# Optimization experiments

Measured on AMD Instinct MI355X. Metric: run time of the kernel, lower is better.

The kernel has to match this reference:

```python
import jax, jax.numpy as jnp
import numpy as np

N_LAYERS = 24  # number of recurrent applications of the shared HashLinear


def setup_inputs() -> dict:
    key = jax.random.key(0)
    ks = jax.random.split(key, 9)
    B, D_IN, N, N_OUT = 1024, 784, 4096, 10
    s_in = 1.0 / np.sqrt(D_IN)
    s_h = 1.0 / np.sqrt(N)
    x = jax.random.normal(ks[0], (B, D_IN), jnp.float32)
    # nn.Linear(prod(input_dim), 2*n_units)
    W_in = jax.random.uniform(ks[1], (2 * N, D_IN), jnp.float32, -s_in, s_in)
    b_in = jax.random.uniform(ks[2], (2 * N,), jnp.float32, -s_in, s_in)
    # HashLinear(n_units, n_units, period=1, 'hash'): learnable +/-1 context key + shared linear
    key_sp = jnp.where(jax.random.bernoulli(ks[3], 0.5, (1, N)), 1.0, -1.0).astype(jnp.float32)
    W_sp = jax.random.uniform(ks[4], (N, N), jnp.float32, -s_h, s_h)
    b_sp = jax.random.uniform(ks[5], (N,), jnp.float32, -s_h, s_h)
    # HashLinear(n_units, 10, period=1, 'hash')
    key_f = jnp.where(jax.random.bernoulli(ks[6], 0.5, (1, N)), 1.0, -1.0).astype(jnp.float32)
    W_f = jax.random.uniform(ks[7], (N_OUT, N), jnp.float32, -s_h, s_h)
    b_f = jax.random.uniform(ks[8], (N_OUT,), jnp.float32, -s_h, s_h)
    return {"x": x, "W_in": W_in, "b_in": b_in, "key_sp": key_sp, "W_sp": W_sp,
            "b_sp": b_sp, "key_f": key_f, "W_f": W_f, "b_f": b_f, "time": 0}


def _hash_linear(xa, xb, o, W, b):
    # Superposition HashLinear: same shared weight applied to both streams,
    # each modulated by the +/-1 context key o ([n_in]).
    ya = (xa * o) @ W.T + b
    yb = (xb * o) @ W.T + b
    return ya, yb


def reference(x, W_in, b_in, key_sp, W_sp, b_sp, key_f, W_f, b_f, time):
    N = W_sp.shape[0]
    r = x @ W_in.T + b_in                 # [B, 2N]
    r_a, r_b = r[:, :N], r[:, N:]         # torch.split(r, n_units, 1)
    pre0 = r_a
    r_a, r_b = jax.nn.relu(r_a), jax.nn.relu(r_b)
    o = key_sp[time % key_sp.shape[0]]    # period=1, time=0 in the module

    def step(carry, _):
        a, b2 = carry
        ya, yb = _hash_linear(a, b2, o, W_sp, b_sp)
        return (jax.nn.relu(ya), jax.nn.relu(yb)), ya  # collect preactivation r_a

    (r_a, r_b), pres = jax.lax.scan(step, (r_a, r_b), None, length=N_LAYERS)
    of = key_f[time % key_f.shape[0]]
    out_a, out_b = _hash_linear(r_a, r_b, of, W_f, b_f)  # [B,10], [B,10]
    preactivations = jnp.concatenate([pre0[None], pres], axis=0)  # [N_LAYERS+1, B, N]
    return (out_a, out_b, preactivations)
```

## Files before the change

### kernel.cpp

```cpp
#include <hip/hip_runtime.h>
#include <hip/hip_bf16.h>
#include <stdint.h>

typedef __bf16 bf16x8 __attribute__((ext_vector_type(8)));
typedef float  f32x4  __attribute__((ext_vector_type(4)));
typedef unsigned short ushort8v __attribute__((ext_vector_type(8)));

#define NH      4096
#define MB      1024
#define M2      2048
#define DIN     784
#define KPAD    832
#define N_IN    8192
#define NLAYERS 24
#define NOUT    10

#define ASL     (128 * 64)
#define SLOT    (2 * ASL)

__device__ __forceinline__ unsigned short f2bf(float x) {
  union { float f; unsigned u; } v; v.f = x;
  unsigned r = v.u + 0x7FFFu + ((v.u >> 16) & 1u);
  return (unsigned short)(r >> 16);
}
__device__ __forceinline__ float bf2f(unsigned short u) {
  union { unsigned u; float f; } v; v.u = ((unsigned)u) << 16; return v.f;
}

__device__ __forceinline__ void async16(const void* g, void* l) {
  __builtin_amdgcn_global_load_lds(
      (const __attribute__((address_space(1))) void*)g,
      (__attribute__((address_space(3))) void*)l, 16, 0, 0);
}

__global__ void k_conv_wsp(const float* __restrict__ W, const float* __restrict__ o,
                           unsigned short* __restrict__ out) {
  size_t i = ((size_t)blockIdx.x * blockDim.x + threadIdx.x) * 4;
  if (i >= (size_t)NH * NH) return;
  float4 w = *reinterpret_cast<const float4*>(W + i);
  int k = (int)(i & (NH - 1));
  float4 ov = *reinterpret_cast<const float4*>(o + k);
  ushort4 r;
  r.x = f2bf(w.x * ov.x); r.y = f2bf(w.y * ov.y);
  r.z = f2bf(w.z * ov.z); r.w = f2bf(w.w * ov.w);
  *reinterpret_cast<ushort4*>(out + i) = r;
}

__global__ void k_conv_pad2(const float* __restrict__ Win, const float* __restrict__ x,
                            unsigned short* __restrict__ Win_bf,
                            unsigned short* __restrict__ X_bf) {
  size_t i = (size_t)blockIdx.x * blockDim.x + threadIdx.x;
  if (i >= (size_t)(N_IN + MB) * KPAD) return;
  int r = (int)(i / KPAD), c = (int)(i % KPAD);
  if (r < N_IN) Win_bf[i] = (c < DIN) ? f2bf(Win[(size_t)r * DIN + c]) : (unsigned short)0;
  else {
    int rr = r - N_IN;
    X_bf[(size_t)rr * KPAD + c] = (c < DIN) ? f2bf(x[(size_t)rr * DIN + c]) : (unsigned short)0;
  }
}

__device__ __forceinline__ void gemm_core(
    const unsigned short* __restrict__ Ag, const unsigned short* __restrict__ Bg,
    int K, int bm, int bn, unsigned short* lds, f32x4 acc[4][4])
{
  const int t    = threadIdx.x;
  const int lane = t & 63;
  const int wave = t >> 6;
  const int wm   = wave >> 1;
  const int wn   = wave & 1;
  const int l15  = lane & 15;
  const int lkb  = (lane >> 4) * 16;

  const int srow = t >> 3;
  const int sb   = ((t & 7) * 16) ^ ((srow & 7) << 4);
  const unsigned aG0 = (unsigned)((bm + srow) * K + (sb >> 1));
  const unsigned bG0 = (unsigned)((bn + srow) * K + (sb >> 1));

  auto STAGE = [&](int bufIdx, int k0) {
    unsigned short* s = lds + bufIdx * SLOT;
#pragma unroll
    for (int j = 0; j < 4; ++j)
      async16(Ag + aG0 + (unsigned)(j * 32 * K + k0), s + t * 8 + j * 2048);
#pragma unroll
    for (int j = 0; j < 4; ++j)
      async16(Bg + bG0 + (unsigned)(j * 32 * K + k0), s + ASL + t * 8 + j * 2048);
  };

  int aRd[2][4], bRd[2][4];
#pragma unroll
  for (int kk = 0; kk < 2; ++kk)
#pragma unroll
    for (int i = 0; i < 4; ++i) {
      const int ra = wm * 64 + i * 16 + l15;
      aRd[kk][i] = (ra * 128 + ((kk * 64 + lkb) ^ ((ra & 7) << 4))) >> 1;
      const int rb = wn * 64 + i * 16 + l15;
      bRd[kk][i] = (rb * 128 + ((kk * 64 + lkb) ^ ((rb & 7) << 4))) >> 1;
    }

  const int nt = K >> 6;
  STAGE(0, 0);
  asm volatile("s_waitcnt vmcnt(0)" ::: "memory");
  __builtin_amdgcn_s_barrier();

  int buf = 0;
  for (int kt = 0; kt < nt; ++kt) {
    const unsigned short* base = lds + buf * SLOT;
    bf16x8 a[2][4], b[2][4];
#pragma unroll
    for (int kk = 0; kk < 2; ++kk) {
#pragma unroll
      for (int i = 0; i < 4; ++i) a[kk][i] = *reinterpret_cast<const bf16x8*>(base + aRd[kk][i]);
#pragma unroll
      for (int i = 0; i < 4; ++i) b[kk][i] = *reinterpret_cast<const bf16x8*>(base + ASL + bRd[kk][i]);
    }
    if (kt + 1 < nt) STAGE(buf ^ 1, (kt + 1) << 6);
    __builtin_amdgcn_s_setprio(1);
#pragma unroll
    for (int kk = 0; kk < 2; ++kk)
#pragma unroll
      for (int mi = 0; mi < 4; ++mi)
#pragma unroll
        for (int ni = 0; ni < 4; ++ni)
          acc[mi][ni] = __builtin_amdgcn_mfma_f32_16x16x32_bf16(a[kk][mi], b[kk][ni], acc[mi][ni], 0, 0, 0);
    __builtin_amdgcn_s_setprio(0);
    if (kt + 1 < nt) {
      asm volatile("s_waitcnt vmcnt(0)" ::: "memory");
      __builtin_amdgcn_s_barrier();
    }
    buf ^= 1;
  }
}

__global__ __launch_bounds__(256, 2) void k_gemm_layer(
    const unsigned short* __restrict__ A, const unsigned short* __restrict__ W,
    const float* __restrict__ bias, float* __restrict__ preact,
    unsigned short* __restrict__ Anext)
{
  __shared__ __align__(16) unsigned short lds[2 * SLOT];
  const int bid = blockIdx.x;
  const int xcd = bid & 7;
  const int idx = bid >> 3;
  const int bm  = (idx >> 2) * 128;
  const int bn  = (xcd * 4 + (idx & 3)) * 128;
  f32x4 acc[4][4] = {};
  gemm_core(A, W, NH, bm, bn, lds, acc);

  const int lane = threadIdx.x & 63;
  const int wave = threadIdx.x >> 6;
  const int wm = (wave >> 1) * 64, wn = (wave & 1) * 64;
  const int l15 = lane & 15;
#pragma unroll
  for (int mi = 0; mi < 4; ++mi) {
    const int gm0 = bm + wm + mi * 16 + (lane >> 4) * 4;
#pragma unroll
    for (int ni = 0; ni < 4; ++ni) {
      const int gn = bn + wn + ni * 16 + l15;
      const float bv = bias[gn];
#pragma unroll
      for (int r = 0; r < 4; ++r) {
        const int gm = gm0 + r;
        const float y = acc[mi][ni][r] + bv;
        if (gm < MB) preact[(size_t)gm * NH + gn] = y;
        Anext[(size_t)gm * NH + gn] = f2bf(y > 0.f ? y : 0.f);
      }
    }
  }
}

__global__ __launch_bounds__(256, 2) void k_gemm_in(
    const unsigned short* __restrict__ X, const unsigned short* __restrict__ W,
    const float* __restrict__ bias, float* __restrict__ preact0,
    unsigned short* __restrict__ A0)
{
  __shared__ __align__(16) unsigned short lds[2 * SLOT];
  const int bid = blockIdx.x;
  const int xcd = bid & 7;
  const int idx = bid >> 3;
  const int bm  = (idx >> 3) * 128;
  const int bn  = (xcd * 8 + (idx & 7)) * 128;
  f32x4 acc[4][4] = {};
  gemm_core(X, W, KPAD, bm, bn, lds, acc);

  const int lane = threadIdx.x & 63;
  const int wave = threadIdx.x >> 6;
  const int wm = (wave >> 1) * 64, wn = (wave & 1) * 64;
  const int l15 = lane & 15;
#pragma unroll
  for (int mi = 0; mi < 4; ++mi) {
    const int gm0 = bm + wm + mi * 16 + (lane >> 4) * 4;
#pragma unroll
    for (int ni = 0; ni < 4; ++ni) {
      const int gn = bn + wn + ni * 16 + l15;
      const float bv = bias[gn];
#pragma unroll
      for (int r = 0; r < 4; ++r) {
        const int gm = gm0 + r;
        const float y = acc[mi][ni][r] + bv;
        const unsigned short rl = f2bf(y > 0.f ? y : 0.f);
        if (gn < NH) {
          preact0[(size_t)gm * NH + gn] = y;
          A0[(size_t)gm * NH + gn] = rl;
        } else {
          A0[(size_t)(MB + gm) * NH + (gn - NH)] = rl;
        }
      }
    }
  }
}

__global__ __launch_bounds__(256) void k_final(
    const unsigned short* __restrict__ A, const float* __restrict__ Wf,
    const float* __restrict__ of, const float* __restrict__ bf_,
    float* __restrict__ out)
{
  __shared__ float red[4][NOUT];
  const int t = threadIdx.x;
  for (int rr = 0; rr < 8; ++rr) {
    const int m = blockIdx.x * 8 + rr;
    float accj[NOUT];
#pragma unroll
    for (int j = 0; j < NOUT; ++j) accj[j] = 0.f;
    for (int k0 = t * 8; k0 < NH; k0 += 256 * 8) {
      const ushort8v av = *reinterpret_cast<const ushort8v*>(A + (size_t)m * NH + k0);
      const float4 o0 = *reinterpret_cast<const float4*>(of + k0);
      const float4 o1 = *reinterpret_cast<const float4*>(of + k0 + 4);
      float a[8];
      a[0] = bf2f(av[0]) * o0.x; a[1] = bf2f(av[1]) * o0.y;
      a[2] = bf2f(av[2]) * o0.z; a[3] = bf2f(av[3]) * o0.w;
      a[4] = bf2f(av[4]) * o1.x; a[5] = bf2f(av[5]) * o1.y;
      a[6] = bf2f(av[6]) * o1.z; a[7] = bf2f(av[7]) * o1.w;
#pragma unroll
      for (int j = 0; j < NOUT; ++j) {
        const float4 w0 = *reinterpret_cast<const float4*>(Wf + (size_t)j * NH + k0);
        const float4 w1 = *reinterpret_cast<const float4*>(Wf + (size_t)j * NH + k0 + 4);
        accj[j] += a[0]*w0.x + a[1]*w0.y + a[2]*w0.z + a[3]*w0.w
                 + a[4]*w1.x + a[5]*w1.y + a[6]*w1.z + a[7]*w1.w;
      }
    }
#pragma unroll
    for (int j = 0; j < NOUT; ++j) {
      float v = accj[j];
      for (int off = 32; off > 0; off >>= 1) v += __shfl_down(v, off);
      if ((t & 63) == 0) red[t >> 6][j] = v;
    }
    __syncthreads();
    if (t < NOUT)
      out[(size_t)m * NOUT + t] = red[0][t] + red[1][t] + red[2][t] + red[3][t] + bf_[t];
    __syncthreads();
  }
}

extern "C" void kernel_launch(void* const* d_in, const int* in_sizes, int n_in,
                              void* d_out, int out_size, void* d_ws, size_t ws_size,
                              hipStream_t stream) {
  const float* x     = (const float*)d_in[0];
  const float* W_in  = (const float*)d_in[1];
  const float* b_in  = (const float*)d_in[2];
  const float* keysp = (const float*)d_in[3];
  const float* W_sp  = (const float*)d_in[4];
  const float* b_sp  = (const float*)d_in[5];
  const float* keyf  = (const float*)d_in[6];
  const float* W_f   = (const float*)d_in[7];
  const float* b_f   = (const float*)d_in[8];

  float* out    = (float*)d_out;
  float* preact = out + (size_t)2 * MB * NOUT;

  char* ws = (char*)d_ws;
  unsigned short* Wsp_bf = (unsigned short*)ws;  ws += (size_t)NH * NH * 2;
  unsigned short* A0     = (unsigned short*)ws;  ws += (size_t)M2 * NH * 2;
  unsigned short* A1     = (unsigned short*)ws;  ws += (size_t)M2 * NH * 2;
  unsigned short* Win_bf = (unsigned short*)ws;  ws += (size_t)N_IN * KPAD * 2;
  unsigned short* X_bf   = (unsigned short*)ws;  ws += (size_t)MB * KPAD * 2;

  k_conv_wsp<<<(NH * (size_t)NH / 4 + 255) / 256, 256, 0, stream>>>(W_sp, keysp, Wsp_bf);
  k_conv_pad2<<<((size_t)(N_IN + MB) * KPAD + 255) / 256, 256, 0, stream>>>(
      W_in, x, Win_bf, X_bf);

  k_gemm_in<<<512, 256, 0, stream>>>(X_bf, Win_bf, b_in, preact, A0);

  unsigned short* Ain = A0;
  unsigned short* Aout = A1;
  for (int tlay = 0; tlay < NLAYERS; ++tlay) {
    float* pre = preact + (size_t)(tlay + 1) * MB * NH;
    k_gemm_layer<<<512, 256, 0, stream>>>(Ain, Wsp_bf, b_sp, pre, Aout);
    unsigned short* tmp = Ain; Ain = Aout; Aout = tmp;
  }

  k_final<<<M2 / 8, 256, 0, stream>>>(Ain, W_f, keyf, b_f, out);
}
```

Before: 1.593 ms.

## Triple-buffer A tile and restructure GEMM pipeline with partial vmcnt waits

Splits the LDS staging into three rotating A slots and two B slots, so the A tile is prefetched two k-steps ahead while B is prefetched one step ahead. The single end-of-iteration full wait is replaced by a wait-then-barrier at the top of each iteration that only blocks on the oldest outstanding loads (vmcnt(4)). The goal is to hide more global-load latency behind the MFMA work. In exchange, LDS per block grows from 64KB to 80KB, which may limit occupancy at two blocks per CU, and the vmcnt counting has to match the issue order exactly to stay correct.

```diff
diff --git a/kernel.cpp b/kernel.cpp
--- a/kernel.cpp
+++ b/kernel.cpp
@@ -15,8 +15,8 @@
 #define NLAYERS 24
 #define NOUT    10
 
-#define ASL     (128 * 64)
-#define SLOT    (2 * ASL)
+#define ASLE    8192
+#define BOFF    (3 * ASLE)
 
 __device__ __forceinline__ unsigned short f2bf(float x) {
   union { float f; unsigned u; } v; v.f = x;
@@ -76,14 +76,17 @@
   const unsigned aG0 = (unsigned)((bm + srow) * K + (sb >> 1));
   const unsigned bG0 = (unsigned)((bn + srow) * K + (sb >> 1));
 
-  auto STAGE = [&](int bufIdx, int k0) {
-    unsigned short* s = lds + bufIdx * SLOT;
+  auto STAGE_A = [&](int sA, int k0) {
+    unsigned short* s = lds + sA * ASLE;
 #pragma unroll
     for (int j = 0; j < 4; ++j)
       async16(Ag + aG0 + (unsigned)(j * 32 * K + k0), s + t * 8 + j * 2048);
+  };
+  auto STAGE_B = [&](int sB, int k0) {
+    unsigned short* s = lds + BOFF + sB * ASLE;
 #pragma unroll
     for (int j = 0; j < 4; ++j)
-      async16(Bg + bG0 + (unsigned)(j * 32 * K + k0), s + ASL + t * 8 + j * 2048);
+      async16(Bg + bG0 + (unsigned)(j * 32 * K + k0), s + t * 8 + j * 2048);
   };
 
   int aRd[2][4], bRd[2][4];
@@ -98,22 +101,27 @@
     }
 
   const int nt = K >> 6;
-  STAGE(0, 0);
-  asm volatile("s_waitcnt vmcnt(0)" ::: "memory");
-  __builtin_amdgcn_s_barrier();
-
-  int buf = 0;
+  STAGE_A(0, 0);
+  STAGE_B(0, 0);
+  if (nt > 1) STAGE_A(1, 64);
+
+  int sA = 0, sA2 = 2, sB = 0;
   for (int kt = 0; kt < nt; ++kt) {
-    const unsigned short* base = lds + buf * SLOT;
+    if (kt + 1 < nt) asm volatile("s_waitcnt vmcnt(4)" ::: "memory");
+    else             asm volatile("s_waitcnt vmcnt(0)" ::: "memory");
+    __builtin_amdgcn_s_barrier();
+    if (kt + 1 < nt) STAGE_B(sB ^ 1, (kt + 1) << 6);
+    if (kt + 2 < nt) STAGE_A(sA2, (kt + 2) << 6);
+    const unsigned short* baseA = lds + sA * ASLE;
+    const unsigned short* baseB = lds + BOFF + sB * ASLE;
     bf16x8 a[2][4], b[2][4];
 #pragma unroll
     for (int kk = 0; kk < 2; ++kk) {
 #pragma unroll
-      for (int i = 0; i < 4; ++i) a[kk][i] = *reinterpret_cast<const bf16x8*>(base + aRd[kk][i]);
-#pragma unroll
-      for (int i = 0; i < 4; ++i) b[kk][i] = *reinterpret_cast<const bf16x8*>(base + ASL + bRd[kk][i]);
-    }
-    if (kt + 1 < nt) STAGE(buf ^ 1, (kt + 1) << 6);
+      for (int i = 0; i < 4; ++i) a[kk][i] = *reinterpret_cast<const bf16x8*>(baseA + aRd[kk][i]);
+#pragma unroll
+      for (int i = 0; i < 4; ++i) b[kk][i] = *reinterpret_cast<const bf16x8*>(baseB + bRd[kk][i]);
+    }
     __builtin_amdgcn_s_setprio(1);
 #pragma unroll
     for (int kk = 0; kk < 2; ++kk)
@@ -123,11 +131,9 @@
         for (int ni = 0; ni < 4; ++ni)
           acc[mi][ni] = __builtin_amdgcn_mfma_f32_16x16x32_bf16(a[kk][mi], b[kk][ni], acc[mi][ni], 0, 0, 0);
     __builtin_amdgcn_s_setprio(0);
-    if (kt + 1 < nt) {
-      asm volatile("s_waitcnt vmcnt(0)" ::: "memory");
-      __builtin_amdgcn_s_barrier();
-    }
-    buf ^= 1;
+    sA  = (sA  == 2) ? 0 : sA  + 1;
+    sA2 = (sA2 == 2) ? 0 : sA2 + 1;
+    sB ^= 1;
   }
 }
 
@@ -136,7 +142,7 @@
     const float* __restrict__ bias, float* __restrict__ preact,
     unsigned short* __restrict__ Anext)
 {
-  __shared__ __align__(16) unsigned short lds[2 * SLOT];
+  __shared__ __align__(16) unsigned short lds[5 * ASLE];
   const int bid = blockIdx.x;
   const int xcd = bid & 7;
   const int idx = bid >> 3;
@@ -172,7 +178,7 @@
     const float* __restrict__ bias, float* __restrict__ preact0,
     unsigned short* __restrict__ A0)
 {
-  __shared__ __align__(16) unsigned short lds[2 * SLOT];
+  __shared__ __align__(16) unsigned short lds[5 * ASLE];
   const int bid = blockIdx.x;
   const int xcd = bid & 7;
   const int idx = bid >> 3;
```

Measured after the change: 1.517 ms, median of 2. 4.8% less time.
